# Kernel tuning notes

Measured on AMD Instinct MI355X. Metric: run time of the kernel, lower is better.

The kernel has to match this reference:

```python
import jax, jax.numpy as jnp
import numpy as np

B, L, TXT, D, NQ, H, DEPTH, MLP = 1024, 77, 768, 512, 64, 8, 3, 1024
HEAD = D // H
SCALE = HEAD ** -0.5  # 0.125 (both CrossAttention and Transformer use head_dim scale)
NEG = -1e9


def _ln(x, s, b, eps=1e-5):
    m = jnp.mean(x, axis=-1, keepdims=True)
    v = jnp.var(x, axis=-1, keepdims=True)
    return (x - m) * jax.lax.rsqrt(v + eps) * s + b


def setup_inputs() -> dict:
    key = jax.random.key(0)
    ks = jax.random.split(key, 32)
    g = lambda i, shape, sc=0.02: (jax.random.normal(ks[i], shape, jnp.float32) * sc)
    inp = {
        'text_embed': jax.random.normal(ks[0], (B, L, TXT), jnp.float32),
        'caption_len': 1 + jax.random.randint(ks[1], (B,), 0, L).astype(jnp.int32),
        'in_w': g(2, (TXT, D)), 'in_b': jnp.zeros((D,), jnp.float32),
        'mq': g(3, (1, NQ, D)),  # motion_query parameter (zeros-init in torch; randn for a non-degenerate baseline)
        'wq': g(4, (D, D)), 'wk': g(5, (D, D)), 'wv': g(6, (D, D)),
        'cproj_w': g(7, (D, D)), 'cproj_b': jnp.zeros((D,), jnp.float32),
        'pos': g(8, (1, NQ, D)),
        'ln1_s': jnp.ones((DEPTH, D), jnp.float32), 'ln1_b': jnp.zeros((DEPTH, D), jnp.float32),
        'qkv_w': g(9, (DEPTH, D, 3 * D)), 'qkv_b': jnp.zeros((DEPTH, 3 * D), jnp.float32),
        'aproj_w': g(10, (DEPTH, D, D)), 'aproj_b': jnp.zeros((DEPTH, D), jnp.float32),
        'ln2_s': jnp.ones((DEPTH, D), jnp.float32), 'ln2_b': jnp.zeros((DEPTH, D), jnp.float32),
        'fc1_w': g(11, (DEPTH, D, MLP)), 'fc1_b': jnp.zeros((DEPTH, MLP), jnp.float32),
        'fc2_w': g(12, (DEPTH, MLP, D)), 'fc2_b': jnp.zeros((DEPTH, D), jnp.float32),
        'lnf_s': jnp.ones((D,), jnp.float32), 'lnf_b': jnp.zeros((D,), jnp.float32),
    }
    return inp


def reference(text_embed, in_w, in_b, mq, wq, wk, wv, cproj_w, cproj_b, pos,
              ln1_s, ln1_b, qkv_w, qkv_b, aproj_w, aproj_b,
              ln2_s, ln2_b, fc1_w, fc1_b, fc2_w, fc2_b, lnf_s, lnf_b,
              caption_len):
    # input_proj
    feat = text_embed @ in_w + in_b  # [B, L, D]
    # Vectorized varlen cross-attention (replaces the per-batch python loop):
    # single-head full-dim attention, exactly as CrossAttention (no head reshape).
    q = (mq @ wq)  # [1, NQ, D]
    k = feat @ wk  # [B, L, D]
    v = feat @ wv  # [B, L, D]
    attn = jnp.einsum('bqd,bld->bql', jnp.broadcast_to(q, (feat.shape[0], NQ, D)), k) * SCALE
    valid = jnp.arange(L)[None, :] < caption_len[:, None]  # [B, L]
    attn = jnp.where(valid[:, None, :], attn, NEG)
    attn = jax.nn.softmax(attn, axis=-1)
    x = jnp.einsum('bql,bld->bqd', attn, v)
    x = x @ cproj_w + cproj_b  # [B, NQ, D]

    # Transformer (pre-LN blocks + pos embed + final norm); dropout/drop_path = eval identity
    x = x + pos
    for i in range(DEPTH):
        y = _ln(x, ln1_s[i], ln1_b[i])
        qkv = y @ qkv_w[i] + qkv_b[i]  # [B, NQ, 3D]
        qh, kh, vh = [t.reshape(x.shape[0], NQ, H, HEAD) for t in jnp.split(qkv, 3, axis=-1)]
        a = jnp.einsum('bqhd,bkhd->bhqk', qh, kh) * SCALE
        a = jax.nn.softmax(a, axis=-1)
        o = jnp.einsum('bhqk,bkhd->bqhd', a, vh).reshape(x.shape[0], NQ, D)
        x = x + (o @ aproj_w[i] + aproj_b[i])
        y = _ln(x, ln2_s[i], ln2_b[i])
        x = x + (jax.nn.gelu(y @ fc1_w[i] + fc1_b[i]) @ fc2_w[i] + fc2_b[i])
    return _ln(x, lnf_s, lnf_b)
```

## Files before the change

kernel.cpp:

```cpp
#include <hip/hip_runtime.h>
#include <hip/hip_bf16.h>

#define B_SZ 1024
#define L_SEQ 77
#define TXT_D 768
#define DM 512
#define NQ 64
#define NH 8
#define HEADD 64
#define DEPTH 3
#define MLP_D 1024
#define ATT_SCALE 0.125f
#define BL_ROWS (B_SZ * L_SEQ)

typedef __attribute__((ext_vector_type(8))) short bf16x8;
typedef __attribute__((ext_vector_type(4))) float f32x4;
typedef __attribute__((ext_vector_type(8))) unsigned short ushort8v;
typedef __attribute__((ext_vector_type(4))) unsigned short ushort4v;

__device__ __forceinline__ float bf2f(unsigned short u) {
    return __uint_as_float(((unsigned)u) << 16);
}
__device__ __forceinline__ unsigned short f2bf(float f) {
    unsigned u = __float_as_uint(f);
    unsigned r = (u + 0x7FFFu + ((u >> 16) & 1u)) >> 16;
    return (unsigned short)r;
}
__device__ __forceinline__ float gelu_tanh(float t) {
    return 0.5f * t * (1.0f + tanhf(0.7978845608028654f * (t + 0.044715f * t * t * t)));
}
__device__ __forceinline__ void gld16(const unsigned short* g, unsigned short* l) {
    __builtin_amdgcn_global_load_lds(
        (const __attribute__((address_space(1))) unsigned int*)g,
        (__attribute__((address_space(3))) unsigned int*)l, 16, 0, 0);
}

template <int EPI, bool OBF>
__global__ __launch_bounds__(256) void gemm_mfma(
    const unsigned short* __restrict__ A,
    const unsigned short* __restrict__ BT,
    const float* __restrict__ bias,
    const float* __restrict__ res,
    float* __restrict__ Cf, unsigned short* __restrict__ Cb,
    int M, int N, int K)
{
    __shared__ __align__(16) unsigned short As[128 * 32];
    __shared__ __align__(16) unsigned short Bs[128 * 32];
    int tid = threadIdx.x;
    int m0 = blockIdx.y * 128, n0 = blockIdx.x * 128;
    int lane = tid & 63, wv = tid >> 6;
    int wr = (wv >> 1) * 64, wc = (wv & 1) * 64;
    int lr = lane & 15, lk = (lane >> 4) * 8;

    f32x4 acc[4][4];
#pragma unroll
    for (int i = 0; i < 4; ++i)
#pragma unroll
        for (int j = 0; j < 4; ++j) acc[i][j] = (f32x4){0.f, 0.f, 0.f, 0.f};

    int segrow = lane >> 2;
    int segcol = (lane & 3) * 8;
    const unsigned short* gA0 = A + (long)(m0 + wv * 16 + segrow) * K + segcol;
    const unsigned short* gA1 = gA0 + 64L * K;
    const unsigned short* gB0 = BT + (long)(n0 + wv * 16 + segrow) * K + segcol;
    const unsigned short* gB1 = gB0 + 64L * K;
    unsigned short* lA0 = &As[wv * 512];
    unsigned short* lA1 = &As[(wv + 4) * 512];
    unsigned short* lB0 = &Bs[wv * 512];
    unsigned short* lB1 = &Bs[(wv + 4) * 512];

    for (int k0 = 0; k0 < K; k0 += 32) {
        __syncthreads();
        gld16(gA0 + k0, lA0);
        gld16(gA1 + k0, lA1);
        gld16(gB0 + k0, lB0);
        gld16(gB1 + k0, lB1);
        __syncthreads();
        bf16x8 af[4], bfr[4];
#pragma unroll
        for (int i = 0; i < 4; ++i) af[i]  = *(const bf16x8*)&As[(wr + i * 16 + lr) * 32 + lk];
#pragma unroll
        for (int j = 0; j < 4; ++j) bfr[j] = *(const bf16x8*)&Bs[(wc + j * 16 + lr) * 32 + lk];
#pragma unroll
        for (int i = 0; i < 4; ++i)
#pragma unroll
            for (int j = 0; j < 4; ++j)
                acc[i][j] = __builtin_amdgcn_mfma_f32_16x16x32_bf16(af[i], bfr[j], acc[i][j], 0, 0, 0);
    }

    int crow = wr + (lane >> 4) * 4;
    int ccol = wc + lr;
#pragma unroll
    for (int j = 0; j < 4; ++j) {
        int n = n0 + ccol + j * 16;
        float bv = bias ? bias[n] : 0.f;
#pragma unroll
        for (int i = 0; i < 4; ++i) {
#pragma unroll
            for (int r = 0; r < 4; ++r) {
                int m = m0 + crow + i * 16 + r;
                float val = acc[i][j][r] + bv;
                if (EPI == 1) val += res[(long)m * N + n];
                if (EPI == 3) val += res[(long)(m & (NQ - 1)) * N + n];
                if (EPI == 2) val = gelu_tanh(val);
                if (EPI == 4) {
                    if (n < 1024) Cb[(long)m * 1024 + n] = f2bf(val);
                    else ((unsigned short*)res)[((long)(m >> 6) * 512 + (n - 1024)) * 64 + (m & 63)] = f2bf(val);
                } else if (OBF) {
                    Cb[(long)m * N + n] = f2bf(val);
                } else {
                    Cf[(long)m * N + n] = val;
                }
            }
        }
    }
}

__global__ __launch_bounds__(256) void self_attn_mfma(
    const unsigned short* __restrict__ qk,
    const unsigned short* __restrict__ vt,
    unsigned short* __restrict__ o)
{
    __shared__ __align__(16) unsigned short p_lds[4][64][68];
    int tid = threadIdx.x, lane = tid & 63, wv = tid >> 6;
    int b = blockIdx.x >> 1;
    int h = (blockIdx.x & 1) * 4 + wv;
    int col0 = h * HEADD;
    int lr = lane & 15, g = lane >> 4, lk = g * 8;

    const unsigned short* qbase = qk + (long)b * 64 * 1024 + col0;
    const unsigned short* kbase = qbase + 512;

    f32x4 s[4][4];
#pragma unroll
    for (int i = 0; i < 4; ++i)
#pragma unroll
        for (int j = 0; j < 4; ++j) s[i][j] = (f32x4){0.f, 0.f, 0.f, 0.f};

#pragma unroll
    for (int ks = 0; ks < 2; ++ks) {
        bf16x8 aq[4], bk[4];
#pragma unroll
        for (int i = 0; i < 4; ++i)
            aq[i] = *(const bf16x8*)(qbase + (long)(i * 16 + lr) * 1024 + ks * 32 + lk);
#pragma unroll
        for (int j = 0; j < 4; ++j)
            bk[j] = *(const bf16x8*)(kbase + (long)(j * 16 + lr) * 1024 + ks * 32 + lk);
#pragma unroll
        for (int i = 0; i < 4; ++i)
#pragma unroll
            for (int j = 0; j < 4; ++j)
                s[i][j] = __builtin_amdgcn_mfma_f32_16x16x32_bf16(aq[i], bk[j], s[i][j], 0, 0, 0);
    }

#pragma unroll
    for (int i = 0; i < 4; ++i) {
#pragma unroll
        for (int r = 0; r < 4; ++r) {
            float m = fmaxf(fmaxf(s[i][0][r], s[i][1][r]), fmaxf(s[i][2][r], s[i][3][r]));
            m = fmaxf(m, __shfl_xor(m, 1, 64));
            m = fmaxf(m, __shfl_xor(m, 2, 64));
            m = fmaxf(m, __shfl_xor(m, 4, 64));
            m = fmaxf(m, __shfl_xor(m, 8, 64));
            float sum = 0.f;
#pragma unroll
            for (int j = 0; j < 4; ++j) {
                float e = __expf(ATT_SCALE * (s[i][j][r] - m));
                s[i][j][r] = e;
                sum += e;
            }
            sum += __shfl_xor(sum, 1, 64);
            sum += __shfl_xor(sum, 2, 64);
            sum += __shfl_xor(sum, 4, 64);
            sum += __shfl_xor(sum, 8, 64);
            float inv = 1.f / sum;
            int row = i * 16 + g * 4 + r;
#pragma unroll
            for (int j = 0; j < 4; ++j)
                p_lds[wv][row][j * 16 + lr] = f2bf(s[i][j][r] * inv);
        }
    }
    __syncthreads();

    f32x4 oa[4][4];
#pragma unroll
    for (int i = 0; i < 4; ++i)
#pragma unroll
        for (int j = 0; j < 4; ++j) oa[i][j] = (f32x4){0.f, 0.f, 0.f, 0.f};

#pragma unroll
    for (int ks = 0; ks < 2; ++ks) {
        bf16x8 ap[4], bv[4];
#pragma unroll
        for (int i = 0; i < 4; ++i)
            ap[i] = *(const bf16x8*)&p_lds[wv][i * 16 + lr][ks * 32 + lk];
#pragma unroll
        for (int j = 0; j < 4; ++j)
            bv[j] = *(const bf16x8*)(vt + ((long)b * 512 + col0 + j * 16 + lr) * 64 + ks * 32 + lk);
#pragma unroll
        for (int i = 0; i < 4; ++i)
#pragma unroll
            for (int j = 0; j < 4; ++j)
                oa[i][j] = __builtin_amdgcn_mfma_f32_16x16x32_bf16(ap[i], bv[j], oa[i][j], 0, 0, 0);
    }

    unsigned short* ob = o + (long)b * 64 * 512 + col0;
#pragma unroll
    for (int i = 0; i < 4; ++i)
#pragma unroll
        for (int j = 0; j < 4; ++j)
#pragma unroll
            for (int r = 0; r < 4; ++r)
                ob[(long)(i * 16 + g * 4 + r) * 512 + j * 16 + lr] = f2bf(oa[i][j][r]);
}

__global__ __launch_bounds__(256) void qk_gemm(
    const unsigned short* __restrict__ A,
    const unsigned short* __restrict__ Bq,
    float* __restrict__ S)
{
    __shared__ __align__(16) unsigned short As[128 * 32];
    __shared__ __align__(16) unsigned short Bs[64 * 32];
    int tid = threadIdx.x, lane = tid & 63, wv = tid >> 6;
    int m0 = blockIdx.x * 128;
    int lr = lane & 15, lk = (lane >> 4) * 8;

    int segrow = lane >> 2, segcol = (lane & 3) * 8;
    const unsigned short* gA0 = A + (long)(m0 + wv * 16 + segrow) * 512 + segcol;
    const unsigned short* gA1 = gA0 + 64L * 512;
    const unsigned short* gB  = Bq + (long)(wv * 16 + segrow) * 512 + segcol;
    unsigned short* lA0 = &As[wv * 512];
    unsigned short* lA1 = &As[(wv + 4) * 512];
    unsigned short* lB  = &Bs[wv * 512];

    f32x4 acc[2][4];
#pragma unroll
    for (int i = 0; i < 2; ++i)
#pragma unroll
        for (int j = 0; j < 4; ++j) acc[i][j] = (f32x4){0.f, 0.f, 0.f, 0.f};

    for (int k0 = 0; k0 < 512; k0 += 32) {
        __syncthreads();
        gld16(gA0 + k0, lA0);
        gld16(gA1 + k0, lA1);
        gld16(gB + k0, lB);
        __syncthreads();
        bf16x8 af[2], bq[4];
#pragma unroll
        for (int i = 0; i < 2; ++i) af[i] = *(const bf16x8*)&As[(wv * 32 + i * 16 + lr) * 32 + lk];
#pragma unroll
        for (int j = 0; j < 4; ++j) bq[j] = *(const bf16x8*)&Bs[(j * 16 + lr) * 32 + lk];
#pragma unroll
        for (int i = 0; i < 2; ++i)
#pragma unroll
            for (int j = 0; j < 4; ++j)
                acc[i][j] = __builtin_amdgcn_mfma_f32_16x16x32_bf16(af[i], bq[j], acc[i][j], 0, 0, 0);
    }
    int crow = (lane >> 4) * 4;
#pragma unroll
    for (int i = 0; i < 2; ++i)
#pragma unroll
        for (int j = 0; j < 4; ++j)
#pragma unroll
            for (int r = 0; r < 4; ++r)
                S[(long)(m0 + wv * 32 + i * 16 + crow + r) * 64 + j * 16 + lr] = acc[i][j][r] * ATT_SCALE;
}

__global__ __launch_bounds__(256) void softmax_kernel(
    const float* __restrict__ S, const int* __restrict__ caplen,
    unsigned short* __restrict__ P)
{
    __shared__ float Sl[77][65];
    __shared__ float red[256];
    __shared__ float gm[64], gi[64];
    int b = blockIdx.x, tid = threadIdx.x;
    int cap = caplen[b];
    for (int i = tid; i < 77 * 16; i += 256) {
        int r = i >> 4, c = (i & 15) << 2;
        *(float4*)&Sl[r][c] = *(const float4*)(S + ((long)b * 77 + r) * 64 + c);
    }
    __syncthreads();
    int q = tid & 63, ch = tid >> 6;
    int l0 = ch * 20;
    int l1 = l0 + 20; if (l1 > 77) l1 = 77;
    int lc = (l1 < cap) ? l1 : cap;
    float m = -1e30f;
    for (int l = l0; l < lc; ++l) m = fmaxf(m, Sl[l][q]);
    red[tid] = m;
    __syncthreads();
    if (tid < 64) gm[tid] = fmaxf(fmaxf(red[tid], red[tid + 64]), fmaxf(red[tid + 128], red[tid + 192]));
    __syncthreads();
    float mq = gm[q];
    float s = 0.f;
    for (int l = l0; l < lc; ++l) s += expf(Sl[l][q] - mq);
    red[tid] = s;
    __syncthreads();
    if (tid < 64) gi[tid] = 1.f / (red[tid] + red[tid + 64] + red[tid + 128] + red[tid + 192]);
    __syncthreads();
    float iq = gi[q];
    unsigned short* Pq = P + ((long)b * 64 + q) * 96;
    int w0 = ch * 24;
    for (int l = w0; l < w0 + 24; ++l) {
        float val = (l < cap) ? expf(Sl[l][q] - mq) * iq : 0.f;
        Pq[l] = f2bf(val);
    }
}

__global__ __launch_bounds__(256) void pv_kernel(
    const unsigned short* __restrict__ P,
    const unsigned short* __restrict__ VT,
    unsigned short* __restrict__ out)
{
    int b = blockIdx.x;
    int tid = threadIdx.x, lane = tid & 63, wv = tid >> 6;
    int lr = lane & 15, lk = (lane >> 4) * 8;
    int wc = wv * 128;

    f32x4 acc[4][8];
#pragma unroll
    for (int i = 0; i < 4; ++i)
#pragma unroll
        for (int j = 0; j < 8; ++j) acc[i][j] = (f32x4){0.f, 0.f, 0.f, 0.f};

    bf16x8 pa[4][3];
#pragma unroll
    for (int rt = 0; rt < 4; ++rt)
#pragma unroll
        for (int ks = 0; ks < 3; ++ks)
            pa[rt][ks] = *(const bf16x8*)(P + ((long)b * 64 + rt * 16 + lr) * 96 + ks * 32 + lk);

    const long col0 = (long)b * 77;
#pragma unroll
    for (int ks = 0; ks < 3; ++ks) {
#pragma unroll
        for (int ct = 0; ct < 8; ++ct) {
            bf16x8 vb = *(const bf16x8*)(VT + (long)(wc + ct * 16 + lr) * BL_ROWS + col0 + ks * 32 + lk);
#pragma unroll
            for (int rt = 0; rt < 4; ++rt)
                acc[rt][ct] = __builtin_amdgcn_mfma_f32_16x16x32_bf16(pa[rt][ks], vb, acc[rt][ct], 0, 0, 0);
        }
    }
    int crow = (lane >> 4) * 4;
#pragma unroll
    for (int rt = 0; rt < 4; ++rt)
#pragma unroll
        for (int ct = 0; ct < 8; ++ct)
#pragma unroll
            for (int r = 0; r < 4; ++r)
                out[(long)(b * 64 + rt * 16 + crow + r) * 512 + wc + ct * 16 + lr] = f2bf(acc[rt][ct][r]);
}

#define BM 64
#define BN 64
#define BK 16
template <int EPI>
__global__ __launch_bounds__(256) void gemm_kernel(
    const float* __restrict__ A, const float* __restrict__ Bm,
    const float* __restrict__ bias, const float* __restrict__ res,
    float* __restrict__ C, int M, int N, int K)
{
    __shared__ float As[BK][BM];
    __shared__ float Bs[BK][BN];
    int tid = threadIdx.x;
    int m0 = blockIdx.y * BM;
    int n0 = blockIdx.x * BN;
    int tx = tid & 15, ty = tid >> 4;

    float acc[4][4] = {};
    int arow = tid >> 2;
    int akk  = (tid & 3) << 2;
    int brow = tid >> 4;
    int bcol = (tid & 15) << 2;

    const float* Aptr = A + (long)(m0 + arow) * K + akk;
    const float* Bptr = Bm + (long)brow * N + n0 + bcol;

    for (int k0 = 0; k0 < K; k0 += BK) {
        float4 av = *(const float4*)(Aptr + k0);
        float4 bv = *(const float4*)(Bptr + (long)k0 * N);
        __syncthreads();
        As[akk + 0][arow] = av.x;
        As[akk + 1][arow] = av.y;
        As[akk + 2][arow] = av.z;
        As[akk + 3][arow] = av.w;
        *(float4*)&Bs[brow][bcol] = bv;
        __syncthreads();
#pragma unroll
        for (int k = 0; k < BK; ++k) {
            float4 a = *(const float4*)&As[k][ty << 2];
            float4 b = *(const float4*)&Bs[k][tx << 2];
            float ar[4] = {a.x, a.y, a.z, a.w};
            float br[4] = {b.x, b.y, b.z, b.w};
#pragma unroll
            for (int i = 0; i < 4; ++i)
#pragma unroll
                for (int j = 0; j < 4; ++j)
                    acc[i][j] += ar[i] * br[j];
        }
    }
#pragma unroll
    for (int i = 0; i < 4; ++i) {
        int m = m0 + (ty << 2) + i;
        float out[4];
#pragma unroll
        for (int j = 0; j < 4; ++j) {
            int n = n0 + (tx << 2) + j;
            float val = acc[i][j];
            if (bias) val += bias[n];
            out[j] = val;
        }
        float4 o4 = {out[0], out[1], out[2], out[3]};
        *(float4*)(C + (long)m * N + n0 + (tx << 2)) = o4;
    }
}

__global__ __launch_bounds__(256) void transpose_w_kernel(
    const float* __restrict__ src, unsigned short* __restrict__ dst,
    int K, int N, long sstride, long dstride)
{
    __shared__ float t[32][33];
    int n0 = blockIdx.x * 32, k0 = blockIdx.y * 32;
    const float* s = src + blockIdx.z * sstride;
    unsigned short* d = dst + blockIdx.z * dstride;
    int tx = threadIdx.x & 31, ty = threadIdx.x >> 5;
#pragma unroll
    for (int r = 0; r < 32; r += 8)
        t[ty + r][tx] = s[(long)(k0 + ty + r) * N + n0 + tx];
    __syncthreads();
#pragma unroll
    for (int r = 0; r < 32; r += 8)
        d[(long)(n0 + ty + r) * K + k0 + tx] = f2bf(t[tx][ty + r]);
}

__global__ __launch_bounds__(256) void cvt_kernel(
    const float* __restrict__ in, unsigned short* __restrict__ out, long n8)
{
    long i = (long)blockIdx.x * 256 + threadIdx.x;
    long stride = (long)gridDim.x * 256;
    for (; i < n8; i += stride) {
        float4 v0 = *(const float4*)(in + i * 8);
        float4 v1 = *(const float4*)(in + i * 8 + 4);
        ushort8v o;
        o[0] = f2bf(v0.x); o[1] = f2bf(v0.y); o[2] = f2bf(v0.z); o[3] = f2bf(v0.w);
        o[4] = f2bf(v1.x); o[5] = f2bf(v1.y); o[6] = f2bf(v1.z); o[7] = f2bf(v1.w);
        *(ushort8v*)(out + i * 8) = o;
    }
}

template <bool OBF>
__global__ __launch_bounds__(256) void ln_kernel(
    const float* __restrict__ x, const float* __restrict__ s,
    const float* __restrict__ b, void* __restrict__ yv, int rows)
{
    int wave = threadIdx.x >> 6;
    int lane = threadIdx.x & 63;
    int row = blockIdx.x * 4 + wave;
    if (row >= rows) return;
    const float* xr = x + (long)row * DM;
    float4 v0 = *(const float4*)(xr + lane * 4);
    float4 v1 = *(const float4*)(xr + 256 + lane * 4);
    float sum = v0.x + v0.y + v0.z + v0.w + v1.x + v1.y + v1.z + v1.w;
    float sq = v0.x * v0.x + v0.y * v0.y + v0.z * v0.z + v0.w * v0.w +
               v1.x * v1.x + v1.y * v1.y + v1.z * v1.z + v1.w * v1.w;
#pragma unroll
    for (int off = 32; off; off >>= 1) {
        sum += __shfl_xor(sum, off, 64);
        sq  += __shfl_xor(sq,  off, 64);
    }
    float mean = sum * (1.0f / DM);
    float var = sq * (1.0f / DM) - mean * mean;
    float rs = rsqrtf(var + 1e-5f);
    int c0 = lane * 4, c1 = 256 + lane * 4;
    float o[8];
    o[0] = (v0.x - mean) * rs * s[c0 + 0] + b[c0 + 0];
    o[1] = (v0.y - mean) * rs * s[c0 + 1] + b[c0 + 1];
    o[2] = (v0.z - mean) * rs * s[c0 + 2] + b[c0 + 2];
    o[3] = (v0.w - mean) * rs * s[c0 + 3] + b[c0 + 3];
    o[4] = (v1.x - mean) * rs * s[c1 + 0] + b[c1 + 0];
    o[5] = (v1.y - mean) * rs * s[c1 + 1] + b[c1 + 1];
    o[6] = (v1.z - mean) * rs * s[c1 + 2] + b[c1 + 2];
    o[7] = (v1.w - mean) * rs * s[c1 + 3] + b[c1 + 3];
    if (OBF) {
        unsigned short* yr = (unsigned short*)yv + (long)row * DM;
        ushort4v p0 = {f2bf(o[0]), f2bf(o[1]), f2bf(o[2]), f2bf(o[3])};
        ushort4v p1 = {f2bf(o[4]), f2bf(o[5]), f2bf(o[6]), f2bf(o[7])};
        *(ushort4v*)(yr + c0) = p0;
        *(ushort4v*)(yr + c1) = p1;
    } else {
        float* yr = (float*)yv + (long)row * DM;
        float4 p0 = {o[0], o[1], o[2], o[3]};
        float4 p1 = {o[4], o[5], o[6], o[7]};
        *(float4*)(yr + c0) = p0;
        *(float4*)(yr + c1) = p1;
    }
}

extern "C" void kernel_launch(void* const* d_in, const int* in_sizes, int n_in,
                              void* d_out, int out_size, void* d_ws, size_t ws_size,
                              hipStream_t stream)
{
    const float* text_embed = (const float*)d_in[0];
    const int*   caption_len = (const int*)d_in[1];
    const float* in_w = (const float*)d_in[2];
    const float* in_b = (const float*)d_in[3];
    const float* mq = (const float*)d_in[4];
    const float* wq = (const float*)d_in[5];
    const float* wk = (const float*)d_in[6];
    const float* wv = (const float*)d_in[7];
    const float* cproj_w = (const float*)d_in[8];
    const float* cproj_b = (const float*)d_in[9];
    const float* pos = (const float*)d_in[10];
    const float* ln1_s = (const float*)d_in[11];
    const float* ln1_b = (const float*)d_in[12];
    const float* qkv_w = (const float*)d_in[13];
    const float* qkv_b = (const float*)d_in[14];
    const float* aproj_w = (const float*)d_in[15];
    const float* aproj_b = (const float*)d_in[16];
    const float* ln2_s = (const float*)d_in[17];
    const float* ln2_b = (const float*)d_in[18];
    const float* fc1_w = (const float*)d_in[19];
    const float* fc1_b = (const float*)d_in[20];
    const float* fc2_w = (const float*)d_in[21];
    const float* fc2_b = (const float*)d_in[22];
    const float* lnf_s = (const float*)d_in[23];
    const float* lnf_b = (const float*)d_in[24];

    const int BL = BL_ROWS;
    const int BQ = B_SZ * NQ;
    const long TE_N = (long)B_SZ * L_SEQ * TXT_D;

    char* w = (char*)d_ws;
    unsigned short* regA = (unsigned short*)w;     w += 201326592;
    unsigned short* feat_bf = (unsigned short*)w;  w += (long)BL * DM * 2;
    unsigned short* kbuf = (unsigned short*)w;     w += (long)BL * DM * 2;
    unsigned short* VT = (unsigned short*)w;       w += (long)BL * DM * 2 + 256;
    unsigned short* ybuf = (unsigned short*)w;     w += (long)BQ * DM * 2;
    float* xbuf = (float*)w;                       w += (long)BQ * DM * 4;
    float* qbuf = (float*)w;                       w += (long)NQ * DM * 4;
    unsigned short* qbf = (unsigned short*)w;      w += (long)NQ * DM * 2;
    unsigned short* wT = (unsigned short*)w;
    unsigned short* in_wT  = wT;
    unsigned short* wkT    = in_wT + 512 * 768;
    unsigned short* wvT    = wkT + 512 * 512;
    unsigned short* cprojT = wvT + 512 * 512;
    unsigned short* qkvT   = cprojT + 512 * 512;
    unsigned short* aprojT = qkvT + 3 * 1536 * 512;
    unsigned short* fc1T   = aprojT + 3 * 512 * 512;
    unsigned short* fc2T   = fc1T + 3 * 1024 * 512;

    unsigned short* te_bf = regA;
    float* S_all = (float*)regA;
    unsigned short* Pbuf = (unsigned short*)((char*)regA + 25165824);
    unsigned short* qkbuf = regA;
    unsigned short* vtbuf = regA + 134217728 / 2;
    unsigned short* hbuf = regA;

    dim3 blk(256);

    transpose_w_kernel<<<dim3(512 / 32, TXT_D / 32, 1), blk, 0, stream>>>(in_w, in_wT, TXT_D, 512, 0, 0);
    transpose_w_kernel<<<dim3(512 / 32, 512 / 32, 1), blk, 0, stream>>>(wk, wkT, 512, 512, 0, 0);
    transpose_w_kernel<<<dim3(512 / 32, 512 / 32, 1), blk, 0, stream>>>(wv, wvT, 512, 512, 0, 0);
    transpose_w_kernel<<<dim3(512 / 32, 512 / 32, 1), blk, 0, stream>>>(cproj_w, cprojT, 512, 512, 0, 0);
    transpose_w_kernel<<<dim3(1536 / 32, 512 / 32, 3), blk, 0, stream>>>(qkv_w, qkvT, 512, 1536, 512L * 1536, 1536L * 512);
    transpose_w_kernel<<<dim3(512 / 32, 512 / 32, 3), blk, 0, stream>>>(aproj_w, aprojT, 512, 512, 512L * 512, 512L * 512);
    transpose_w_kernel<<<dim3(1024 / 32, 512 / 32, 3), blk, 0, stream>>>(fc1_w, fc1T, 512, 1024, 512L * 1024, 1024L * 512);
    transpose_w_kernel<<<dim3(512 / 32, 1024 / 32, 3), blk, 0, stream>>>(fc2_w, fc2T, 1024, 512, 1024L * 512, 512L * 1024);
    cvt_kernel<<<dim3(2048), blk, 0, stream>>>(text_embed, te_bf, TE_N / 8);
    gemm_kernel<0><<<dim3(DM / BN, 1), blk, 0, stream>>>(mq, wq, nullptr, nullptr, qbuf, NQ, DM, DM);
    cvt_kernel<<<dim3(16), blk, 0, stream>>>(qbuf, qbf, (long)NQ * DM / 8);

    gemm_mfma<0, true><<<dim3(DM / 128, BL / 128), blk, 0, stream>>>(
        te_bf, in_wT, in_b, nullptr, nullptr, feat_bf, BL, DM, TXT_D);
    gemm_mfma<0, true><<<dim3(DM / 128, BL / 128), blk, 0, stream>>>(
        feat_bf, wkT, nullptr, nullptr, nullptr, kbuf, BL, DM, DM);
    gemm_mfma<0, true><<<dim3(BL / 128, DM / 128), blk, 0, stream>>>(
        wvT, feat_bf, nullptr, nullptr, nullptr, VT, DM, BL, DM);
    qk_gemm<<<dim3(BL / 128), blk, 0, stream>>>(kbuf, qbf, S_all);
    softmax_kernel<<<dim3(B_SZ), blk, 0, stream>>>(S_all, caption_len, Pbuf);
    pv_kernel<<<dim3(B_SZ), blk, 0, stream>>>(Pbuf, VT, ybuf);
    gemm_mfma<3, false><<<dim3(DM / 128, BQ / 128), blk, 0, stream>>>(
        ybuf, cprojT, cproj_b, pos, xbuf, nullptr, BQ, DM, DM);

    for (int i = 0; i < DEPTH; ++i) {
        ln_kernel<true><<<dim3(BQ / 4), blk, 0, stream>>>(
            xbuf, ln1_s + i * DM, ln1_b + i * DM, ybuf, BQ);
        gemm_mfma<4, true><<<dim3(3 * DM / 128, BQ / 128), blk, 0, stream>>>(
            ybuf, qkvT + (long)i * 1536 * 512, qkv_b + i * 3 * DM, (const float*)vtbuf,
            nullptr, qkbuf, BQ, 3 * DM, DM);
        self_attn_mfma<<<dim3(B_SZ * 2), blk, 0, stream>>>(qkbuf, vtbuf, ybuf);
        gemm_mfma<1, false><<<dim3(DM / 128, BQ / 128), blk, 0, stream>>>(
            ybuf, aprojT + (long)i * 512 * 512, aproj_b + i * DM, xbuf,
            xbuf, nullptr, BQ, DM, DM);
        ln_kernel<true><<<dim3(BQ / 4), blk, 0, stream>>>(
            xbuf, ln2_s + i * DM, ln2_b + i * DM, ybuf, BQ);
        gemm_mfma<2, true><<<dim3(MLP_D / 128, BQ / 128), blk, 0, stream>>>(
            ybuf, fc1T + (long)i * 1024 * 512, fc1_b + i * MLP_D, nullptr,
            nullptr, hbuf, BQ, MLP_D, DM);
        gemm_mfma<1, false><<<dim3(DM / 128, BQ / 128), blk, 0, stream>>>(
            hbuf, fc2T + (long)i * 512 * 1024, fc2_b + i * DM, xbuf,
            xbuf, nullptr, BQ, DM, MLP_D);
    }
    ln_kernel<false><<<dim3(BQ / 4), blk, 0, stream>>>(
        xbuf, lnf_s, lnf_b, (float*)d_out, BQ);
}
```

Measured before the change: 3.260 ms.

## Replace GEMM with 256x256-tile, 4-stage pipelined, XCD-swizzled MFMA kernel

```diff
diff --git a/kernel.cpp b/kernel.cpp
--- a/kernel.cpp
+++ b/kernel.cpp
@@ -36,7 +36,7 @@
 }
 
 template <int EPI, bool OBF>
-__global__ __launch_bounds__(256) void gemm_mfma(
+__global__ __launch_bounds__(512, 2) void gemm256(
     const unsigned short* __restrict__ A,
     const unsigned short* __restrict__ BT,
     const float* __restrict__ bias,
@@ -44,72 +44,103 @@
     float* __restrict__ Cf, unsigned short* __restrict__ Cb,
     int M, int N, int K)
 {
-    __shared__ __align__(16) unsigned short As[128 * 32];
-    __shared__ __align__(16) unsigned short Bs[128 * 32];
+    __shared__ __align__(16) unsigned short ldsA[4][8192];
+    __shared__ __align__(16) unsigned short ldsB[4][8192];
+
     int tid = threadIdx.x;
-    int m0 = blockIdx.y * 128, n0 = blockIdx.x * 128;
-    int lane = tid & 63, wv = tid >> 6;
-    int wr = (wv >> 1) * 64, wc = (wv & 1) * 64;
-    int lr = lane & 15, lk = (lane >> 4) * 8;
-
-    f32x4 acc[4][4];
-#pragma unroll
-    for (int i = 0; i < 4; ++i)
-#pragma unroll
-        for (int j = 0; j < 4; ++j) acc[i][j] = (f32x4){0.f, 0.f, 0.f, 0.f};
-
-    int segrow = lane >> 2;
-    int segcol = (lane & 3) * 8;
-    const unsigned short* gA0 = A + (long)(m0 + wv * 16 + segrow) * K + segcol;
-    const unsigned short* gA1 = gA0 + 64L * K;
-    const unsigned short* gB0 = BT + (long)(n0 + wv * 16 + segrow) * K + segcol;
-    const unsigned short* gB1 = gB0 + 64L * K;
-    unsigned short* lA0 = &As[wv * 512];
-    unsigned short* lA1 = &As[(wv + 4) * 512];
-    unsigned short* lB0 = &Bs[wv * 512];
-    unsigned short* lB1 = &Bs[(wv + 4) * 512];
-
-    for (int k0 = 0; k0 < K; k0 += 32) {
-        __syncthreads();
-        gld16(gA0 + k0, lA0);
-        gld16(gA1 + k0, lA1);
-        gld16(gB0 + k0, lB0);
-        gld16(gB1 + k0, lB1);
-        __syncthreads();
-        bf16x8 af[4], bfr[4];
-#pragma unroll
-        for (int i = 0; i < 4; ++i) af[i]  = *(const bf16x8*)&As[(wr + i * 16 + lr) * 32 + lk];
-#pragma unroll
-        for (int j = 0; j < 4; ++j) bfr[j] = *(const bf16x8*)&Bs[(wc + j * 16 + lr) * 32 + lk];
-#pragma unroll
-        for (int i = 0; i < 4; ++i)
-#pragma unroll
-            for (int j = 0; j < 4; ++j)
-                acc[i][j] = __builtin_amdgcn_mfma_f32_16x16x32_bf16(af[i], bfr[j], acc[i][j], 0, 0, 0);
-    }
-
-    int crow = wr + (lane >> 4) * 4;
-    int ccol = wc + lr;
-#pragma unroll
-    for (int j = 0; j < 4; ++j) {
-        int n = n0 + ccol + j * 16;
-        float bv = bias ? bias[n] : 0.f;
-#pragma unroll
-        for (int i = 0; i < 4; ++i) {
+    int lane = tid & 63, wid = tid >> 6;
+    int wr = wid >> 2, wc = wid & 3;
+    int lr = lane & 15, hi = lane >> 4;
+
+    int nwg = gridDim.x, id = blockIdx.x;
+    int xq = nwg >> 3, xr = nwg & 7;
+    int xcd = id & 7, lid = id >> 3;
+    int wg = (xcd < xr ? xcd * (xq + 1) : xr * (xq + 1) + (xcd - xr) * xq) + lid;
+    int nbn = N >> 8;
+    int m0 = (wg / nbn) << 8, n0 = (wg % nbn) << 8;
+
+    int r0 = tid >> 2;
+    int gc = (tid & 3) * 8;
+    const unsigned short* gA = A  + (long)(m0 + r0) * K + gc;
+    const unsigned short* gB = BT + (long)(n0 + r0) * K + gc;
+    const long rowK128 = 128L * (long)K;
+    int dstb = wid * 512;
+
+    int abase = (wr * 128 + lr) * 32 + hi * 8;
+    int bbase = (wc * 64 + lr) * 32 + hi * 8;
+
+    f32x4 acc[8][4];
+#pragma unroll
+    for (int m = 0; m < 8; ++m)
+#pragma unroll
+        for (int n = 0; n < 4; ++n) acc[m][n] = (f32x4){0.f, 0.f, 0.f, 0.f};
+
+    const int T = K >> 5;
+
+#define STAGE(kt) { \
+    int q_ = (kt) & 3; \
+    const unsigned short* ga_ = gA + (long)(kt) * 32; \
+    const unsigned short* gb_ = gB + (long)(kt) * 32; \
+    gld16(ga_,           &ldsA[q_][dstb]); \
+    gld16(ga_ + rowK128, &ldsA[q_][dstb + 4096]); \
+    gld16(gb_,           &ldsB[q_][dstb]); \
+    gld16(gb_ + rowK128, &ldsB[q_][dstb + 4096]); }
+
+#define COMPUTE(t) { \
+    int q_ = (t) & 3; \
+    bf16x8 bfr_[4]; \
+    _Pragma("unroll") \
+    for (int n = 0; n < 4; ++n) bfr_[n] = *(const bf16x8*)&ldsB[q_][bbase + n * 512]; \
+    __builtin_amdgcn_s_setprio(1); \
+    _Pragma("unroll") \
+    for (int m = 0; m < 8; ++m) { \
+        bf16x8 af_ = *(const bf16x8*)&ldsA[q_][abase + m * 512]; \
+        _Pragma("unroll") \
+        for (int n = 0; n < 4; ++n) \
+            acc[m][n] = __builtin_amdgcn_mfma_f32_16x16x32_bf16(af_, bfr_[n], acc[m][n], 0, 0, 0); \
+    } \
+    __builtin_amdgcn_s_setprio(0); }
+
+#define GITER(t, NCNT, DOSTAGE) { \
+    asm volatile("s_waitcnt vmcnt(" #NCNT ")" ::: "memory"); \
+    __builtin_amdgcn_s_barrier(); \
+    __builtin_amdgcn_sched_barrier(0); \
+    if (DOSTAGE) STAGE((t) + 3); \
+    COMPUTE(t); }
+
+    STAGE(0); STAGE(1); STAGE(2);
+
+    int t = 0;
+    for (; t < T - 3; ++t) GITER(t, 8, true);
+    GITER(T - 3, 8, false);
+    GITER(T - 2, 4, false);
+    GITER(T - 1, 0, false);
+
+#undef GITER
+#undef COMPUTE
+#undef STAGE
+
+    int r4 = hi * 4;
+#pragma unroll
+    for (int n = 0; n < 4; ++n) {
+        int col = n0 + wc * 64 + n * 16 + lr;
+        float bv = bias ? bias[col] : 0.f;
+#pragma unroll
+        for (int m = 0; m < 8; ++m) {
 #pragma unroll
             for (int r = 0; r < 4; ++r) {
-                int m = m0 + crow + i * 16 + r;
-                float val = acc[i][j][r] + bv;
-                if (EPI == 1) val += res[(long)m * N + n];
-                if (EPI == 3) val += res[(long)(m & (NQ - 1)) * N + n];
+                int row = m0 + wr * 128 + m * 16 + r4 + r;
+                float val = acc[m][n][r] + bv;
+                if (EPI == 1) val += res[(long)row * N + col];
+                if (EPI == 3) val += res[(long)(row & (NQ - 1)) * N + col];
                 if (EPI == 2) val = gelu_tanh(val);
                 if (EPI == 4) {
-                    if (n < 1024) Cb[(long)m * 1024 + n] = f2bf(val);
-                    else ((unsigned short*)res)[((long)(m >> 6) * 512 + (n - 1024)) * 64 + (m & 63)] = f2bf(val);
+                    if (col < 1024) Cb[(long)row * 1024 + col] = f2bf(val);
+                    else ((unsigned short*)res)[((long)(row >> 6) * 512 + (col - 1024)) * 64 + (row & 63)] = f2bf(val);
                 } else if (OBF) {
-                    Cb[(long)m * N + n] = f2bf(val);
+                    Cb[(long)row * N + col] = f2bf(val);
                 } else {
-                    Cf[(long)m * N + n] = val;
+                    Cf[(long)row * N + col] = val;
                 }
             }
         }
@@ -555,7 +586,7 @@
     unsigned short* vtbuf = regA + 134217728 / 2;
     unsigned short* hbuf = regA;
 
-    dim3 blk(256);
+    dim3 blk(256), blk2(512);
 
     transpose_w_kernel<<<dim3(512 / 32, TXT_D / 32, 1), blk, 0, stream>>>(in_w, in_wT, TXT_D, 512, 0, 0);
     transpose_w_kernel<<<dim3(512 / 32, 512 / 32, 1), blk, 0, stream>>>(wk, wkT, 512, 512, 0, 0);
@@ -569,34 +600,34 @@
     gemm_kernel<0><<<dim3(DM / BN, 1), blk, 0, stream>>>(mq, wq, nullptr, nullptr, qbuf, NQ, DM, DM);
     cvt_kernel<<<dim3(16), blk, 0, stream>>>(qbuf, qbf, (long)NQ * DM / 8);
 
-    gemm_mfma<0, true><<<dim3(DM / 128, BL / 128), blk, 0, stream>>>(
+    gemm256<0, true><<<dim3((BL / 256) * (DM / 256)), blk2, 0, stream>>>(
         te_bf, in_wT, in_b, nullptr, nullptr, feat_bf, BL, DM, TXT_D);
-    gemm_mfma<0, true><<<dim3(DM / 128, BL / 128), blk, 0, stream>>>(
+    gemm256<0, true><<<dim3((BL / 256) * (DM / 256)), blk2, 0, stream>>>(
         feat_bf, wkT, nullptr, nullptr, nullptr, kbuf, BL, DM, DM);
-    gemm_mfma<0, true><<<dim3(BL / 128, DM / 128), blk, 0, stream>>>(
+    gemm256<0, true><<<dim3((DM / 256) * (BL / 256)), blk2, 0, stream>>>(
         wvT, feat_bf, nullptr, nullptr, nullptr, VT, DM, BL, DM);
     qk_gemm<<<dim3(BL / 128), blk, 0, stream>>>(kbuf, qbf, S_all);
     softmax_kernel<<<dim3(B_SZ), blk, 0, stream>>>(S_all, caption_len, Pbuf);
     pv_kernel<<<dim3(B_SZ), blk, 0, stream>>>(Pbuf, VT, ybuf);
-    gemm_mfma<3, false><<<dim3(DM / 128, BQ / 128), blk, 0, stream>>>(
+    gemm256<3, false><<<dim3((BQ / 256) * (DM / 256)), blk2, 0, stream>>>(
         ybuf, cprojT, cproj_b, pos, xbuf, nullptr, BQ, DM, DM);
 
     for (int i = 0; i < DEPTH; ++i) {
         ln_kernel<true><<<dim3(BQ / 4), blk, 0, stream>>>(
             xbuf, ln1_s + i * DM, ln1_b + i * DM, ybuf, BQ);
-        gemm_mfma<4, true><<<dim3(3 * DM / 128, BQ / 128), blk, 0, stream>>>(
+        gemm256<4, true><<<dim3((BQ / 256) * (3 * DM / 256)), blk2, 0, stream>>>(
             ybuf, qkvT + (long)i * 1536 * 512, qkv_b + i * 3 * DM, (const float*)vtbuf,
             nullptr, qkbuf, BQ, 3 * DM, DM);
         self_attn_mfma<<<dim3(B_SZ * 2), blk, 0, stream>>>(qkbuf, vtbuf, ybuf);
-        gemm_mfma<1, false><<<dim3(DM / 128, BQ / 128), blk, 0, stream>>>(
+        gemm256<1, false><<<dim3((BQ / 256) * (DM / 256)), blk2, 0, stream>>>(
             ybuf, aprojT + (long)i * 512 * 512, aproj_b + i * DM, xbuf,
             xbuf, nullptr, BQ, DM, DM);
         ln_kernel<true><<<dim3(BQ / 4), blk, 0, stream>>>(
             xbuf, ln2_s + i * DM, ln2_b + i * DM, ybuf, BQ);
-        gemm_mfma<2, true><<<dim3(MLP_D / 128, BQ / 128), blk, 0, stream>>>(
+        gemm256<2, true><<<dim3((BQ / 256) * (MLP_D / 256)), blk2, 0, stream>>>(
             ybuf, fc1T + (long)i * 1024 * 512, fc1_b + i * MLP_D, nullptr,
             nullptr, hbuf, BQ, MLP_D, DM);
-        gemm_mfma<1, false><<<dim3(DM / 128, BQ / 128), blk, 0, stream>>>(
+        gemm256<1, false><<<dim3((BQ / 256) * (DM / 256)), blk2, 0, stream>>>(
             hbuf, fc2T + (long)i * 512 * 1024, fc2_b + i * DM, xbuf,
             xbuf, nullptr, BQ, DM, MLP_D);
     }
```

Result: slower. 3.949 ms (+21.1%).

## Double-buffer LDS tiles in MFMA GEMM to overlap loads with compute

Applied to the files above, without the earlier changes.

```diff
diff --git a/kernel.cpp b/kernel.cpp
--- a/kernel.cpp
+++ b/kernel.cpp
@@ -44,8 +44,8 @@
     float* __restrict__ Cf, unsigned short* __restrict__ Cb,
     int M, int N, int K)
 {
-    __shared__ __align__(16) unsigned short As[128 * 32];
-    __shared__ __align__(16) unsigned short Bs[128 * 32];
+    __shared__ __align__(16) unsigned short As[2][4096];
+    __shared__ __align__(16) unsigned short Bs[2][4096];
     int tid = threadIdx.x;
     int m0 = blockIdx.y * 128, n0 = blockIdx.x * 128;
     int lane = tid & 63, wv = tid >> 6;
@@ -64,29 +64,37 @@
     const unsigned short* gA1 = gA0 + 64L * K;
     const unsigned short* gB0 = BT + (long)(n0 + wv * 16 + segrow) * K + segcol;
     const unsigned short* gB1 = gB0 + 64L * K;
-    unsigned short* lA0 = &As[wv * 512];
-    unsigned short* lA1 = &As[(wv + 4) * 512];
-    unsigned short* lB0 = &Bs[wv * 512];
-    unsigned short* lB1 = &Bs[(wv + 4) * 512];
-
-    for (int k0 = 0; k0 < K; k0 += 32) {
+
+#define STAGE(kt, q) { \
+    gld16(gA0 + (long)(kt) * 32, &As[q][wv * 512]); \
+    gld16(gA1 + (long)(kt) * 32, &As[q][(wv + 4) * 512]); \
+    gld16(gB0 + (long)(kt) * 32, &Bs[q][wv * 512]); \
+    gld16(gB1 + (long)(kt) * 32, &Bs[q][(wv + 4) * 512]); }
+
+#define COMPUTE(q) { \
+    bf16x8 af_[4], bf_[4]; \
+    _Pragma("unroll") \
+    for (int i = 0; i < 4; ++i) af_[i] = *(const bf16x8*)&As[q][(wr + i * 16 + lr) * 32 + lk]; \
+    _Pragma("unroll") \
+    for (int j = 0; j < 4; ++j) bf_[j] = *(const bf16x8*)&Bs[q][(wc + j * 16 + lr) * 32 + lk]; \
+    _Pragma("unroll") \
+    for (int i = 0; i < 4; ++i) \
+        _Pragma("unroll") \
+        for (int j = 0; j < 4; ++j) \
+            acc[i][j] = __builtin_amdgcn_mfma_f32_16x16x32_bf16(af_[i], bf_[j], acc[i][j], 0, 0, 0); }
+
+    const int T = K >> 5;
+    STAGE(0, 0);
+    __syncthreads();
+    for (int t = 0; t < T - 1; ++t) {
+        STAGE(t + 1, (t + 1) & 1);
+        COMPUTE(t & 1);
         __syncthreads();
-        gld16(gA0 + k0, lA0);
-        gld16(gA1 + k0, lA1);
-        gld16(gB0 + k0, lB0);
-        gld16(gB1 + k0, lB1);
-        __syncthreads();
-        bf16x8 af[4], bfr[4];
-#pragma unroll
-        for (int i = 0; i < 4; ++i) af[i]  = *(const bf16x8*)&As[(wr + i * 16 + lr) * 32 + lk];
-#pragma unroll
-        for (int j = 0; j < 4; ++j) bfr[j] = *(const bf16x8*)&Bs[(wc + j * 16 + lr) * 32 + lk];
-#pragma unroll
-        for (int i = 0; i < 4; ++i)
-#pragma unroll
-            for (int j = 0; j < 4; ++j)
-                acc[i][j] = __builtin_amdgcn_mfma_f32_16x16x32_bf16(af[i], bfr[j], acc[i][j], 0, 0, 0);
-    }
+    }
+    COMPUTE((T - 1) & 1);
+
+#undef STAGE
+#undef COMPUTE
 
     int crow = wr + (lane >> 4) * 4;
     int ccol = wc + lr;
```

New measurement: 3.161 ms. -3.0%, faster.
